# Performance work log

Hardware: AMD Instinct MI355X
Metric: run time of the kernel (lower is better)

## Reference

```python
import jax, jax.numpy as jnp
import numpy as np

# NVFP4 (e2m1) 4-bit codebook: sign bit in the high position of the nibble
_NVFP4_CODE = jnp.array([0.0, 0.5, 1.0, 1.5, 2.0, 3.0, 4.0, 6.0,
                         -0.0, -0.5, -1.0, -1.5, -2.0, -3.0, -4.0, -6.0],
                        dtype=jnp.float32)

M = 4096          # tokens (batch*seq)
K = 4096          # in_features
N_NVFP4 = 2048
N_FP8 = 1024
N_FP16 = 1024
N = N_NVFP4 + N_FP8 + N_FP16  # out_features
BLOCK = 16        # NVFP4 scale block size along K


def setup_inputs() -> dict:
    key = jax.random.key(0)
    ks = jax.random.split(key, 8)
    x = jax.random.normal(ks[0], (M, K), dtype=jnp.float32)
    nvfp4_idx = jax.random.randint(ks[1], (N_NVFP4, K), 0, 16, dtype=jnp.int32)
    nvfp4_scales = jax.random.uniform(ks[2], (N_NVFP4, K // BLOCK), dtype=jnp.float32) * 0.5 + 0.05
    nvfp4_global_scale = jax.random.uniform(ks[3], (1,), dtype=jnp.float32) * 0.5 + 0.5
    w_fp8 = jax.random.normal(ks[4], (N_FP8, K), dtype=jnp.float32)
    fp8_scale = jax.random.uniform(ks[5], (1,), dtype=jnp.float32) * 0.1 + 0.01
    w_fp16 = jax.random.normal(ks[6], (N_FP16, K), dtype=jnp.float32) * 0.02
    bias = jax.random.normal(ks[7], (N,), dtype=jnp.float32) * 0.01
    inv_perm = jax.random.permutation(jax.random.fold_in(key, 99), N).astype(jnp.int64)
    return {"x": x, "nvfp4_idx": nvfp4_idx, "nvfp4_scales": nvfp4_scales,
            "nvfp4_global_scale": nvfp4_global_scale, "w_fp8": w_fp8,
            "fp8_scale": fp8_scale, "w_fp16": w_fp16, "bias": bias,
            "inv_perm": inv_perm}


def reference(x, nvfp4_idx, nvfp4_scales, nvfp4_global_scale,
              w_fp8, fp8_scale, w_fp16, bias, inv_perm):
    # --- NVFP4 group: dequantize 4-bit codes with per-16-block fp8 scales + global scale
    codes = _NVFP4_CODE[nvfp4_idx]                                   # [n_nvfp4, K]
    scales_full = jnp.repeat(nvfp4_scales, BLOCK, axis=1)            # [n_nvfp4, K]
    w_nvfp4 = codes * scales_full * nvfp4_global_scale[0]            # [n_nvfp4, K]
    y_nvfp4 = jnp.einsum('mk,nk->mn', x, w_nvfp4)                    # [M, n_nvfp4]
    # --- FP8 group: per-tensor scale
    y_fp8 = jnp.einsum('mk,nk->mn', x, w_fp8) * fp8_scale[0]         # [M, n_fp8]
    # --- FP16 group: plain GEMM
    y_fp16 = jnp.einsum('mk,nk->mn', x, w_fp16)                      # [M, n_fp16]
    # --- Reassemble in original channel order via inverse permutation
    y_grouped = jnp.concatenate([y_nvfp4, y_fp8, y_fp16], axis=-1)   # [M, N]
    y = jnp.take(y_grouped, inv_perm, axis=-1)
    return y + bias
```

## Files before the change

### kernel.cpp

```cpp
#include <hip/hip_runtime.h>

#define M_DIM 4096
#define N_DIM 4096
#define K_DIM 4096

typedef float f32x4 __attribute__((ext_vector_type(4)));
typedef __bf16 bf16x8 __attribute__((ext_vector_type(8)));

__device__ __forceinline__ unsigned short f2b(float f) {
    unsigned int u = __float_as_uint(f);
    u += 0x7fffu + ((u >> 16) & 1u);
    return (unsigned short)(u >> 16);
}

__device__ __forceinline__ float nvfp4_decode(int n) {
    unsigned m = (unsigned)n & 7u;
    unsigned e = m >> 1, f = m & 1u;
    unsigned bits = (m >= 2u) ? (((126u + e) << 23) | (f << 22))
                              : (m * 0x3f000000u);
    bits |= ((unsigned)n & 8u) << 28;
    return __uint_as_float(bits);
}

__global__ __launch_bounds__(256) void prep_kernel(
        const float* __restrict__ x, unsigned short* __restrict__ xb,
        const int* __restrict__ idx4, const float* __restrict__ sc4,
        const float* __restrict__ gs4, const float* __restrict__ w8,
        const float* __restrict__ s8, const float* __restrict__ w16,
        const int* __restrict__ iperm, unsigned short* __restrict__ W) {
    const int b = blockIdx.x;
    if (b < 8192) {
        size_t i = ((size_t)b * 256 + threadIdx.x) * 8;
        float4 a0 = *(const float4*)(x + i);
        float4 a1 = *(const float4*)(x + i + 4);
        union { unsigned short h[8]; uint4 u; } o;
        o.h[0] = f2b(a0.x); o.h[1] = f2b(a0.y); o.h[2] = f2b(a0.z); o.h[3] = f2b(a0.w);
        o.h[4] = f2b(a1.x); o.h[5] = f2b(a1.y); o.h[6] = f2b(a1.z); o.h[7] = f2b(a1.w);
        *(uint4*)(xb + i) = o.u;
        return;
    }
    const int j = b - 8192;
    const int t = threadIdx.x;
    const int g = iperm[j];

#pragma unroll
    for (int h = 0; h < 2; ++h) {
        const int k0 = h * 2048 + t * 8;
        union { unsigned short hh[8]; uint4 u; } o;
        if (g < 2048) {
            const float s = sc4[(size_t)g * (K_DIM / 16) + (k0 >> 4)] * gs4[0];
            const int4* ip = (const int4*)(idx4 + (size_t)g * K_DIM + k0);
            int4 v0 = ip[0], v1 = ip[1];
            o.hh[0] = f2b(nvfp4_decode(v0.x) * s);
            o.hh[1] = f2b(nvfp4_decode(v0.y) * s);
            o.hh[2] = f2b(nvfp4_decode(v0.z) * s);
            o.hh[3] = f2b(nvfp4_decode(v0.w) * s);
            o.hh[4] = f2b(nvfp4_decode(v1.x) * s);
            o.hh[5] = f2b(nvfp4_decode(v1.y) * s);
            o.hh[6] = f2b(nvfp4_decode(v1.z) * s);
            o.hh[7] = f2b(nvfp4_decode(v1.w) * s);
        } else if (g < 3072) {
            const float s = s8[0];
            const float4* wp = (const float4*)(w8 + (size_t)(g - 2048) * K_DIM + k0);
            float4 v0 = wp[0], v1 = wp[1];
            o.hh[0] = f2b(v0.x * s); o.hh[1] = f2b(v0.y * s);
            o.hh[2] = f2b(v0.z * s); o.hh[3] = f2b(v0.w * s);
            o.hh[4] = f2b(v1.x * s); o.hh[5] = f2b(v1.y * s);
            o.hh[6] = f2b(v1.z * s); o.hh[7] = f2b(v1.w * s);
        } else {
            const float4* wp = (const float4*)(w16 + (size_t)(g - 3072) * K_DIM + k0);
            float4 v0 = wp[0], v1 = wp[1];
            o.hh[0] = f2b(v0.x); o.hh[1] = f2b(v0.y);
            o.hh[2] = f2b(v0.z); o.hh[3] = f2b(v0.w);
            o.hh[4] = f2b(v1.x); o.hh[5] = f2b(v1.y);
            o.hh[6] = f2b(v1.z); o.hh[7] = f2b(v1.w);
        }
        *(uint4*)(W + (size_t)j * K_DIM + k0) = o.u;
    }
}

#define GLOAD_LDS16(g, l)                                                     \
    __builtin_amdgcn_global_load_lds(                                         \
        (const __attribute__((address_space(1))) void*)(unsigned long long)(g),\
        (__attribute__((address_space(3))) void*)(unsigned int)(unsigned long long)(l), \
        16, 0, 0)

__global__ __launch_bounds__(256) void gemm_kernel(
        const unsigned short* __restrict__ X, const unsigned short* __restrict__ W,
        const float* __restrict__ bias, float* __restrict__ C) {
    __shared__ __align__(16) unsigned short As[128 * 32];
    __shared__ __align__(16) unsigned short Bs[128 * 32];

    const int pid = blockIdx.x;
    const int GROUP = 8;
    const int group_sz = GROUP * (N_DIM / 128);
    const int grp = pid / group_sz;
    const int rem = pid % group_sz;
    const int bm = grp * GROUP + (rem % GROUP);
    const int bn = rem / GROUP;
    const int m0 = bm * 128;
    const int n0 = bn * 128;

    const int tid  = threadIdx.x;
    const int wave = tid >> 6;
    const int lane = tid & 63;
    const int quad = lane >> 4;
    const int l16  = lane & 15;
    const int wr   = wave >> 1;
    const int wc   = wave & 1;

    const int c0 = wave * 64 + lane;
    const int c1 = c0 + 256;
    const int rA0 = c0 >> 2, kcs0 = ((c0 & 3) ^ ((rA0 >> 1) & 3)) * 8;
    const int rA1 = c1 >> 2, kcs1 = ((c1 & 3) ^ ((rA1 >> 1) & 3)) * 8;

    const unsigned short* Xa0 = X + (size_t)(m0 + rA0) * K_DIM + kcs0;
    const unsigned short* Xa1 = X + (size_t)(m0 + rA1) * K_DIM + kcs1;
    const unsigned short* Wb0 = W + (size_t)(n0 + rA0) * K_DIM + kcs0;
    const unsigned short* Wb1 = W + (size_t)(n0 + rA1) * K_DIM + kcs1;

    const int pcr = (quad ^ ((l16 >> 1) & 3)) * 8;

    f32x4 acc[4][4] = {};

    for (int kt = 0; kt < K_DIM / 32; ++kt) {
        const int k0 = kt * 32;
        GLOAD_LDS16(Xa0 + k0, &As[c0 * 8]);
        GLOAD_LDS16(Xa1 + k0, &As[c1 * 8]);
        GLOAD_LDS16(Wb0 + k0, &Bs[c0 * 8]);
        GLOAD_LDS16(Wb1 + k0, &Bs[c1 * 8]);
        __syncthreads();

        bf16x8 af[4], bq[4];
#pragma unroll
        for (int i = 0; i < 4; ++i)
            af[i] = *(const bf16x8*)&As[(wr * 64 + i * 16 + l16) * 32 + pcr];
#pragma unroll
        for (int jj = 0; jj < 4; ++jj)
            bq[jj] = *(const bf16x8*)&Bs[(wc * 64 + jj * 16 + l16) * 32 + pcr];

#pragma unroll
        for (int i = 0; i < 4; ++i)
#pragma unroll
            for (int jj = 0; jj < 4; ++jj)
                acc[i][jj] = __builtin_amdgcn_mfma_f32_16x16x32_bf16(
                    af[i], bq[jj], acc[i][jj], 0, 0, 0);

        __syncthreads();
    }

#pragma unroll
    for (int jj = 0; jj < 4; ++jj) {
        const int col = n0 + wc * 64 + jj * 16 + l16;
        const float bv = bias[col];
#pragma unroll
        for (int i = 0; i < 4; ++i) {
            const int rowb = m0 + wr * 64 + i * 16 + quad * 4;
#pragma unroll
            for (int r = 0; r < 4; ++r)
                C[(size_t)(rowb + r) * N_DIM + col] = acc[i][jj][r] + bv;
        }
    }
}

extern "C" void kernel_launch(void* const* d_in, const int* in_sizes, int n_in,
                              void* d_out, int out_size, void* d_ws, size_t ws_size,
                              hipStream_t stream) {
    const float* x            = (const float*)d_in[0];
    const int*   nvfp4_idx    = (const int*)d_in[1];
    const float* nvfp4_scales = (const float*)d_in[2];
    const float* gscale       = (const float*)d_in[3];
    const float* w_fp8        = (const float*)d_in[4];
    const float* fp8_scale    = (const float*)d_in[5];
    const float* w_fp16       = (const float*)d_in[6];
    const float* bias         = (const float*)d_in[7];
    const int*   inv_perm     = (const int*)d_in[8];
    float* out = (float*)d_out;

    unsigned short* xb = (unsigned short*)d_ws;
    unsigned short* wb = xb + (size_t)M_DIM * K_DIM;

    prep_kernel<<<8192 + 4096, 256, 0, stream>>>(x, xb, nvfp4_idx, nvfp4_scales,
                                                 gscale, w_fp8, fp8_scale, w_fp16,
                                                 inv_perm, wb);
    gemm_kernel<<<(M_DIM / 128) * (N_DIM / 128), 256, 0, stream>>>(xb, wb, bias, out);
}
```

Baseline: 366.5 us.

## Rewrite GEMM as 256x256 tile, 8-wave, double-buffered pipelined kernel

Replaces the 128x128 single-stage bf16 GEMM with a 256x256 tile, 512-thread kernel. It uses 128KB of LDS split into two buffers, with global-to-LDS prefetch interleaved between MFMA quadrants, explicit barriers and waitcnts, and s_setprio around the MFMA bursts. It also changes the tile-to-XCD mapping and splits the prep kernel into separate x-conversion and weight-build kernels. The aim is to raise arithmetic intensity and hide memory latency. The cost is a hand-scheduled pipeline with fragile synchronisation and only 256 workgroups.

```diff
diff --git a/kernel.cpp b/kernel.cpp
--- a/kernel.cpp
+++ b/kernel.cpp
@@ -22,24 +22,23 @@
     return __uint_as_float(bits);
 }
 
-__global__ __launch_bounds__(256) void prep_kernel(
-        const float* __restrict__ x, unsigned short* __restrict__ xb,
+__global__ __launch_bounds__(256) void xconv_kernel(
+        const float* __restrict__ x, unsigned short* __restrict__ xb) {
+    size_t i = ((size_t)blockIdx.x * 256 + threadIdx.x) * 8;
+    float4 a0 = *(const float4*)(x + i);
+    float4 a1 = *(const float4*)(x + i + 4);
+    union { unsigned short h[8]; uint4 u; } o;
+    o.h[0] = f2b(a0.x); o.h[1] = f2b(a0.y); o.h[2] = f2b(a0.z); o.h[3] = f2b(a0.w);
+    o.h[4] = f2b(a1.x); o.h[5] = f2b(a1.y); o.h[6] = f2b(a1.z); o.h[7] = f2b(a1.w);
+    *(uint4*)(xb + i) = o.u;
+}
+
+__global__ __launch_bounds__(256) void wbuild_kernel(
         const int* __restrict__ idx4, const float* __restrict__ sc4,
         const float* __restrict__ gs4, const float* __restrict__ w8,
         const float* __restrict__ s8, const float* __restrict__ w16,
         const int* __restrict__ iperm, unsigned short* __restrict__ W) {
-    const int b = blockIdx.x;
-    if (b < 8192) {
-        size_t i = ((size_t)b * 256 + threadIdx.x) * 8;
-        float4 a0 = *(const float4*)(x + i);
-        float4 a1 = *(const float4*)(x + i + 4);
-        union { unsigned short h[8]; uint4 u; } o;
-        o.h[0] = f2b(a0.x); o.h[1] = f2b(a0.y); o.h[2] = f2b(a0.z); o.h[3] = f2b(a0.w);
-        o.h[4] = f2b(a1.x); o.h[5] = f2b(a1.y); o.h[6] = f2b(a1.z); o.h[7] = f2b(a1.w);
-        *(uint4*)(xb + i) = o.u;
-        return;
-    }
-    const int j = b - 8192;
+    const int j = blockIdx.x;
     const int t = threadIdx.x;
     const int g = iperm[j];
 
@@ -85,80 +84,154 @@
         (__attribute__((address_space(3))) void*)(unsigned int)(unsigned long long)(l), \
         16, 0, 0)
 
-__global__ __launch_bounds__(256) void gemm_kernel(
+#define STAGE(p, d, kt, buf) do {                                             \
+    const unsigned short* _s = (p) + (size_t)(kt) * 64;                       \
+    GLOAD_LDS16(_s,      smem + (buf) * 32768 + (d));                         \
+    GLOAD_LDS16(_s + 32, smem + (buf) * 32768 + (d) + 1024);                  \
+} while (0)
+
+#define LOAD_A(buf, qm) do {                                                  \
+    _Pragma("unroll") for (int mi = 0; mi < 4; ++mi)                          \
+        _Pragma("unroll") for (int kk = 0; kk < 2; ++kk)                      \
+            af[mi][kk] = *(const bf16x8*)(rdA + (buf) * 32768 +               \
+                                          (((qm) * 8 + mi * 2 + kk) << 10));  \
+} while (0)
+
+#define LOAD_B(buf, qn) do {                                                  \
+    _Pragma("unroll") for (int nj = 0; nj < 2; ++nj)                          \
+        _Pragma("unroll") for (int kk = 0; kk < 2; ++kk)                      \
+            bq[nj][kk] = *(const bf16x8*)(rdB + (buf) * 32768 +               \
+                                          (((qn) * 4 + nj * 2 + kk) << 10));  \
+} while (0)
+
+#define MMA(qm, qn) do {                                                      \
+    _Pragma("unroll") for (int mi = 0; mi < 4; ++mi)                          \
+        _Pragma("unroll") for (int nj = 0; nj < 2; ++nj) {                    \
+            acc[(qm)*4+mi][(qn)*2+nj] = __builtin_amdgcn_mfma_f32_16x16x32_bf16( \
+                af[mi][0], bq[nj][0], acc[(qm)*4+mi][(qn)*2+nj], 0, 0, 0);    \
+            acc[(qm)*4+mi][(qn)*2+nj] = __builtin_amdgcn_mfma_f32_16x16x32_bf16( \
+                af[mi][1], bq[nj][1], acc[(qm)*4+mi][(qn)*2+nj], 0, 0, 0);    \
+        }                                                                     \
+} while (0)
+
+#define BARRIER __builtin_amdgcn_s_barrier()
+#define WAIT_LGKM asm volatile("s_waitcnt lgkmcnt(0)" ::: "memory")
+#define WAIT_VM4 asm volatile("s_waitcnt vmcnt(4)" ::: "memory")
+#define PRIO1 __builtin_amdgcn_s_setprio(1)
+#define PRIO0 __builtin_amdgcn_s_setprio(0)
+
+__global__ __launch_bounds__(512, 2) void gemm_kernel(
         const unsigned short* __restrict__ X, const unsigned short* __restrict__ W,
         const float* __restrict__ bias, float* __restrict__ C) {
-    __shared__ __align__(16) unsigned short As[128 * 32];
-    __shared__ __align__(16) unsigned short Bs[128 * 32];
+    __shared__ __align__(128) unsigned char smem[131072];
 
     const int pid = blockIdx.x;
-    const int GROUP = 8;
-    const int group_sz = GROUP * (N_DIM / 128);
-    const int grp = pid / group_sz;
-    const int rem = pid % group_sz;
-    const int bm = grp * GROUP + (rem % GROUP);
-    const int bn = rem / GROUP;
-    const int m0 = bm * 128;
-    const int n0 = bn * 128;
+    const int wg = (pid & 7) * 32 + (pid >> 3);
+    const int bm = wg >> 4, bn = wg & 15;
+    const int m0 = bm * 256, n0 = bn * 256;
 
     const int tid  = threadIdx.x;
     const int wave = tid >> 6;
     const int lane = tid & 63;
+    const int wr   = wave >> 2;
+    const int wc   = wave & 3;
+    const int l16  = lane & 15;
     const int quad = lane >> 4;
-    const int l16  = lane & 15;
-    const int wr   = wave >> 1;
-    const int wc   = wave & 1;
-
-    const int c0 = wave * 64 + lane;
-    const int c1 = c0 + 256;
-    const int rA0 = c0 >> 2, kcs0 = ((c0 & 3) ^ ((rA0 >> 1) & 3)) * 8;
-    const int rA1 = c1 >> 2, kcs1 = ((c1 & 3) ^ ((rA1 >> 1) & 3)) * 8;
-
-    const unsigned short* Xa0 = X + (size_t)(m0 + rA0) * K_DIM + kcs0;
-    const unsigned short* Xa1 = X + (size_t)(m0 + rA1) * K_DIM + kcs1;
-    const unsigned short* Wb0 = W + (size_t)(n0 + rA0) * K_DIM + kcs0;
-    const unsigned short* Wb1 = W + (size_t)(n0 + rA1) * K_DIM + kcs1;
-
-    const int pcr = (quad ^ ((l16 >> 1) & 3)) * 8;
-
-    f32x4 acc[4][4] = {};
-
-    for (int kt = 0; kt < K_DIM / 32; ++kt) {
-        const int k0 = kt * 32;
-        GLOAD_LDS16(Xa0 + k0, &As[c0 * 8]);
-        GLOAD_LDS16(Xa1 + k0, &As[c1 * 8]);
-        GLOAD_LDS16(Wb0 + k0, &Bs[c0 * 8]);
-        GLOAD_LDS16(Wb1 + k0, &Bs[c1 * 8]);
-        __syncthreads();
-
-        bf16x8 af[4], bq[4];
-#pragma unroll
-        for (int i = 0; i < 4; ++i)
-            af[i] = *(const bf16x8*)&As[(wr * 64 + i * 16 + l16) * 32 + pcr];
-#pragma unroll
-        for (int jj = 0; jj < 4; ++jj)
-            bq[jj] = *(const bf16x8*)&Bs[(wc * 64 + jj * 16 + l16) * 32 + pcr];
-
-#pragma unroll
-        for (int i = 0; i < 4; ++i)
-#pragma unroll
-            for (int jj = 0; jj < 4; ++jj)
-                acc[i][jj] = __builtin_amdgcn_mfma_f32_16x16x32_bf16(
-                    af[i], bq[jj], acc[i][jj], 0, 0, 0);
-
-        __syncthreads();
+
+    const int srow = lane >> 2;
+    const int scol = ((lane & 3) ^ ((lane >> 5) << 1)) << 3;
+
+    const unsigned short* pA0 = X + (size_t)(m0 + (wr * 8 + wc) * 16 + srow) * K_DIM + scol;
+    const unsigned short* pA1 = pA0 + (size_t)64 * K_DIM;
+    const unsigned short* pB0 = W + (size_t)(n0 + (wc * 4 + wr) * 16 + srow) * K_DIM + scol;
+    const unsigned short* pB1 = pB0 + (size_t)32 * K_DIM;
+
+    const int dA0 = (((wr * 8 + wc) * 2) << 10) + lane * 16;
+    const int dA1 = dA0 + 8192;
+    const int dB0 = 65536 + (((wc * 4 + wr) * 2) << 10) + lane * 16;
+    const int dB1 = dB0 + 4096;
+
+    const int inner_rd = ((l16 << 6) | (quad << 4)) ^ ((l16 & 8) << 2);
+    const unsigned char* rdA = smem + ((wr * 16) << 10) + inner_rd;
+    const unsigned char* rdB = smem + 65536 + ((wc * 8) << 10) + inner_rd;
+
+    f32x4 acc[8][4] = {};
+    bf16x8 af[4][2], bq[2][2];
+
+    STAGE(pA0, dA0, 0, 0);
+    STAGE(pB0, dB0, 0, 0);
+    STAGE(pB1, dB1, 0, 0);
+    STAGE(pA1, dA1, 0, 0);
+    STAGE(pA0, dA0, 1, 1);
+    STAGE(pB1, dB1, 1, 1);
+    WAIT_VM4;
+    BARRIER;
+
+#pragma unroll 1
+    for (int it = 0; it < 32; ++it) {
+        const int t1 = 2 * it + 1;
+        const int t2 = (2 * it + 2) & 63;
+        const int t3 = (2 * it + 3) & 63;
+
+        LOAD_A(0, 0); LOAD_B(0, 0);
+        STAGE(pB0, dB0, t1, 1);
+        BARRIER; WAIT_LGKM;
+        PRIO1; MMA(0, 0); PRIO0;
+        BARRIER;
+        LOAD_B(0, 1);
+        STAGE(pA1, dA1, t1, 1);
+        BARRIER; WAIT_LGKM;
+        PRIO1; MMA(0, 1); PRIO0;
+        BARRIER;
+        LOAD_A(0, 1);
+        STAGE(pA0, dA0, t2, 0);
+        BARRIER; WAIT_LGKM;
+        PRIO1; MMA(1, 1); PRIO0;
+        BARRIER;
+        LOAD_B(0, 0);
+        STAGE(pB1, dB1, t2, 0);
+        BARRIER; WAIT_LGKM;
+        PRIO1; MMA(1, 0); PRIO0;
+        WAIT_VM4;
+        BARRIER;
+
+        LOAD_A(1, 0); LOAD_B(1, 0);
+        STAGE(pB0, dB0, t2, 0);
+        BARRIER; WAIT_LGKM;
+        PRIO1; MMA(0, 0); PRIO0;
+        BARRIER;
+        LOAD_B(1, 1);
+        STAGE(pA1, dA1, t2, 0);
+        BARRIER; WAIT_LGKM;
+        PRIO1; MMA(0, 1); PRIO0;
+        BARRIER;
+        LOAD_A(1, 1);
+        STAGE(pA0, dA0, t3, 1);
+        BARRIER; WAIT_LGKM;
+        PRIO1; MMA(1, 1); PRIO0;
+        BARRIER;
+        LOAD_B(1, 0);
+        STAGE(pB1, dB1, t3, 1);
+        BARRIER; WAIT_LGKM;
+        PRIO1; MMA(1, 0); PRIO0;
+        WAIT_VM4;
+        BARRIER;
     }
 
-#pragma unroll
-    for (int jj = 0; jj < 4; ++jj) {
-        const int col = n0 + wc * 64 + jj * 16 + l16;
-        const float bv = bias[col];
-#pragma unroll
-        for (int i = 0; i < 4; ++i) {
-            const int rowb = m0 + wr * 64 + i * 16 + quad * 4;
+    const int crow0 = m0 + wr * 128 + quad * 4;
+    const int ccol0 = n0 + wc * 64 + l16;
+    float bv[4];
+#pragma unroll
+    for (int p = 0; p < 4; ++p) bv[p] = bias[ccol0 + p * 16];
+#pragma unroll
+    for (int q = 0; q < 8; ++q) {
+#pragma unroll
+        for (int p = 0; p < 4; ++p) {
+            const int col = ccol0 + p * 16;
+            const int row = crow0 + q * 16;
 #pragma unroll
             for (int r = 0; r < 4; ++r)
-                C[(size_t)(rowb + r) * N_DIM + col] = acc[i][jj][r] + bv;
+                C[(size_t)(row + r) * N_DIM + col] = acc[q][p][r] + bv[p];
         }
     }
 }
@@ -180,8 +253,9 @@
     unsigned short* xb = (unsigned short*)d_ws;
     unsigned short* wb = xb + (size_t)M_DIM * K_DIM;
 
-    prep_kernel<<<8192 + 4096, 256, 0, stream>>>(x, xb, nvfp4_idx, nvfp4_scales,
-                                                 gscale, w_fp8, fp8_scale, w_fp16,
-                                                 inv_perm, wb);
-    gemm_kernel<<<(M_DIM / 128) * (N_DIM / 128), 256, 0, stream>>>(xb, wb, bias, out);
-}
+    xconv_kernel<<<8192, 256, 0, stream>>>(x, xb);
+    wbuild_kernel<<<4096, 256, 0, stream>>>(nvfp4_idx, nvfp4_scales, gscale,
+                                            w_fp8, fp8_scale, w_fp16,
+                                            inv_perm, wb);
+    gemm_kernel<<<(M_DIM / 256) * (N_DIM / 256), 512, 0, stream>>>(xb, wb, bias, out);
+}
```

After: 295.8 us. 19.3% less time.
